# Kernel optimization log

Measured on AMD Instinct MI355X. Metric: run time of the kernel, lower is better.

## Reference

```python
import jax, jax.numpy as jnp
import numpy as np

D_EMBED = 1024
N_HEADS = 16
D_HEAD = 64
D_MLP = 4096
SEQ = 2048
BATCH = 2
ALPHA = 1.0


def setup_inputs() -> dict:
    key = jax.random.key(0)
    ks = jax.random.split(key, 7)
    s = ALPHA / np.sqrt(D_EMBED)
    return {
        "x": jax.random.normal(ks[0], (BATCH, SEQ, D_EMBED), jnp.float32),
        "W_K": s * jax.random.normal(ks[1], (N_HEADS, D_HEAD, D_EMBED), jnp.float32),
        "W_Q": s * jax.random.normal(ks[2], (N_HEADS, D_HEAD, D_EMBED), jnp.float32),
        "W_V": s * jax.random.normal(ks[3], (N_HEADS, D_HEAD, D_EMBED), jnp.float32),
        "W_O": s * jax.random.normal(ks[4], (D_EMBED, N_HEADS * D_HEAD), jnp.float32),
        "W_in": s * jax.random.normal(ks[5], (D_MLP, D_EMBED), jnp.float32),
        "b_in": jnp.zeros((D_MLP,), jnp.float32),
        "W_out": s * jax.random.normal(ks[6], (D_EMBED, D_MLP), jnp.float32),
        "b_out": jnp.zeros((D_EMBED,), jnp.float32),
    }


def reference(x, W_K, W_Q, W_V, W_O, W_in, b_in, W_out, b_out):
    b, c_len, _ = x.shape
    d_head = W_K.shape[1]
    # q/k/v: [batch, head, ctx, d_head]
    k = jnp.einsum('ahe,bce->bach', W_K, x)
    q = jnp.einsum('ahe,bce->bach', W_Q, x)
    v = jnp.einsum('ahe,bce->bach', W_V, x)
    # scores[b,a,c,C] = k_c . q_C  (faithful to original index convention)
    scores = jnp.einsum('bach,baCh->bacC', k, q)
    mask = jnp.tril(jnp.ones((c_len, c_len), dtype=x.dtype))  # [c, C]
    masked = scores * mask - 1e10 * (1.0 - mask)
    attn = jax.nn.softmax(masked / np.sqrt(d_head), axis=-1)  # softmax over C (query idx)
    # z[b,a,C,h] = sum_c v[b,a,c,h] * attn[b,a,c,C]
    z = jnp.einsum('bach,bacC->baCh', v, attn)
    z_flat = jnp.transpose(z, (0, 2, 1, 3)).reshape(b, c_len, -1)  # [b, c, a*h]
    attn_out = jnp.einsum('ef,bcf->bce', W_O, z_flat)
    x = x + attn_out
    h = jnp.einsum('me,bce->bcm', W_in, x) + b_in
    h = jax.nn.relu(h)
    mlp_out = jnp.einsum('em,bcm->bce', W_out, h) + b_out
    return x + mlp_out
```

## Files before the change

kernel.cpp:

```cpp
#include <hip/hip_runtime.h>
#include <hip/hip_bf16.h>
#include <cstdint>
#include <cstddef>

typedef __bf16 bf16;
typedef bf16 bf16x4 __attribute__((ext_vector_type(4)));
typedef bf16 bf16x8 __attribute__((ext_vector_type(8)));
typedef float floatx4 __attribute__((ext_vector_type(4)));
typedef float floatx16 __attribute__((ext_vector_type(16)));
typedef unsigned int uint;

#define MFMA16(a, b, c) __builtin_amdgcn_mfma_f32_16x16x32_bf16((a), (b), (c), 0, 0, 0)
#define MFMA32(a, b, c) __builtin_amdgcn_mfma_f32_32x32x16_bf16((a), (b), (c), 0, 0, 0)

#define K2 0.18033688011112042f

__device__ __forceinline__ void async16(const void* g, void* l) {
    __builtin_amdgcn_global_load_lds((const __attribute__((address_space(1))) void*)g,
                                     (__attribute__((address_space(3))) void*)l,
                                     16, 0, 0);
}

__device__ __forceinline__ void stage64s(const bf16* g0, int ldg, bf16* lds, int wave, int lane) {
#pragma unroll
    for (int i = 0; i < 2; ++i) {
        int r0 = wave * 16 + i * 8;
        async16(g0 + (size_t)(r0 + (lane >> 3)) * ldg + ((lane & 7) ^ (lane >> 3)) * 8,
                lds + r0 * 64);
    }
}
__device__ __forceinline__ void stage64q(const bf16* g0, int ldg, bf16* lds, int wave, int lane) {
    int r0 = wave * 8;
    async16(g0 + (size_t)(r0 + (lane >> 3)) * ldg + ((lane & 7) ^ (lane >> 3)) * 8,
            lds + r0 * 64);
}
__device__ __forceinline__ bf16x8 rd64(const bf16* t, int row, int chunk) {
    return *(const bf16x8*)&t[row * 64 + ((chunk ^ (row & 7)) * 8)];
}
__device__ __forceinline__ bf16x8 rd32(const bf16* t, int row, int quad) {
    return *(const bf16x8*)&t[row * 32 + ((quad ^ (row & 3)) * 8)];
}

__device__ __forceinline__ uint pk2(float lo, float hi) {
    union { bf16 h[2]; uint u; } c;
    c.h[0] = (bf16)lo;
    c.h[1] = (bf16)hi;
    return c.u;
}

__global__ __launch_bounds__(256) void cvt_all(const float* __restrict__ x,
                                               const float* __restrict__ WQ,
                                               const float* __restrict__ WK,
                                               const float* __restrict__ WV,
                                               const float* __restrict__ WO,
                                               const float* __restrict__ Win,
                                               const float* __restrict__ Wout,
                                               bf16* __restrict__ xb,
                                               bf16* __restrict__ wqkv,
                                               bf16* __restrict__ wo,
                                               bf16* __restrict__ win,
                                               bf16* __restrict__ wout) {
    int blk = blockIdx.x;
    const float* src;
    bf16* dst;
    int off;
    if (blk < 1024)      { src = WQ;   dst = wqkv;           off = blk; }
    else if (blk < 2048) { src = WK;   dst = wqkv + 1048576; off = blk - 1024; }
    else if (blk < 3072) { src = WV;   dst = wqkv + 2097152; off = blk - 2048; }
    else if (blk < 4096) { src = WO;   dst = wo;             off = blk - 3072; }
    else if (blk < 8192) { src = Win;  dst = win;            off = blk - 4096; }
    else if (blk < 12288){ src = Wout; dst = wout;           off = blk - 8192; }
    else                 { src = x;    dst = xb;             off = blk - 12288; }
    int i = off * 1024 + threadIdx.x * 4;
    float4 v = *(const float4*)(src + i);
    bf16x4 o = {(bf16)v.x, (bf16)v.y, (bf16)v.z, (bf16)v.w};
    *(bf16x4*)(dst + i) = o;
}

template <int EPI, int NACC>
__device__ __forceinline__ void epilogue(floatx4 (&acc)[4][NACC], int m0, int n0,
                                         int wm, int wn, int col, int quad,
                                         float* Cf, bf16* Cb, int ldc,
                                         const float* bias, const float* res) {
#pragma unroll
    for (int mi = 0; mi < 4; ++mi)
#pragma unroll
        for (int ni = 0; ni < NACC; ++ni)
#pragma unroll
            for (int r = 0; r < 4; ++r) {
                int row = m0 + wm + mi * 16 + quad * 4 + r;
                int cc = n0 + wn + ni * 16 + col;
                size_t idx = (size_t)row * ldc + cc;
                float v = acc[mi][ni][r];
                if constexpr (EPI == 0) {
                    Cb[idx] = (bf16)v;
                } else if constexpr (EPI == 1) {
                    v += res[idx];
                    Cf[idx] = v;
                    Cb[idx] = (bf16)v;
                } else if constexpr (EPI == 2) {
                    v += bias[cc];
                    v = fmaxf(v, 0.f);
                    Cb[idx] = (bf16)v;
                } else {
                    v += bias[cc] + Cf[idx];
                    Cf[idx] = v;
                }
            }
}

template <int EPI>
__global__ __launch_bounds__(256) void gemm_pipe(const bf16* __restrict__ A, int lda,
                                                 const bf16* __restrict__ B, int ldb, int K,
                                                 float* __restrict__ Cf, bf16* __restrict__ Cb,
                                                 int ldc, const float* __restrict__ bias,
                                                 const float* __restrict__ res) {
    __shared__ __align__(16) bf16 As[3][128 * 32];
    __shared__ __align__(16) bf16 Bs[3][128 * 32];
    const int tid = threadIdx.x, wave = tid >> 6, lane = tid & 63;
    const int m0 = blockIdx.y * 128, n0 = blockIdx.x * 128;
    const int wm = (wave >> 1) * 64, wn = (wave & 1) * 64;
    const int col = lane & 15, quad = lane >> 4;
    const int cs8 = ((lane & 3) ^ ((lane >> 2) & 3)) * 8;

    floatx4 acc[4][4];
#pragma unroll
    for (int mi = 0; mi < 4; ++mi)
#pragma unroll
        for (int ni = 0; ni < 4; ++ni) acc[mi][ni] = (floatx4){0.f, 0.f, 0.f, 0.f};

    auto stage = [&](int buf, int k0) {
#pragma unroll
        for (int i = 0; i < 2; ++i) {
            int r0 = wave * 32 + i * 16;
            async16(A + (size_t)(m0 + r0 + (lane >> 2)) * lda + k0 + cs8,
                    As[buf] + r0 * 32);
            async16(B + (size_t)(n0 + r0 + (lane >> 2)) * ldb + k0 + cs8,
                    Bs[buf] + r0 * 32);
        }
    };

    const int nk = K / 32;
    stage(0, 0);
    stage(1, 32);
    for (int it = 0; it < nk; ++it) {
        if (it + 1 < nk) asm volatile("s_waitcnt vmcnt(4)" ::: "memory");
        else             asm volatile("s_waitcnt vmcnt(0)" ::: "memory");
        __builtin_amdgcn_s_barrier();
        if (it + 2 < nk) stage((it + 2) % 3, (it + 2) * 32);

        const bf16* as = As[it % 3];
        const bf16* bs = Bs[it % 3];
        bf16x8 af[4], bfr[4];
#pragma unroll
        for (int mi = 0; mi < 4; ++mi) af[mi] = rd32(as, wm + mi * 16 + col, quad);
#pragma unroll
        for (int ni = 0; ni < 4; ++ni) bfr[ni] = rd32(bs, wn + ni * 16 + col, quad);
#pragma unroll
        for (int mi = 0; mi < 4; ++mi)
#pragma unroll
            for (int ni = 0; ni < 4; ++ni)
                acc[mi][ni] = MFMA16(af[mi], bfr[ni], acc[mi][ni]);
    }
    epilogue<EPI, 4>(acc, m0, n0, wm, wn, col, quad, Cf, Cb, ldc, bias, res);
}

template <int EPI>
__global__ __launch_bounds__(256) void gemm_pipe64(const bf16* __restrict__ A, int lda,
                                                   const bf16* __restrict__ B, int ldb, int K,
                                                   float* __restrict__ Cf, bf16* __restrict__ Cb,
                                                   int ldc, const float* __restrict__ bias,
                                                   const float* __restrict__ res) {
    __shared__ __align__(16) bf16 As[3][128 * 64];
    __shared__ __align__(16) bf16 Bs[3][64 * 64];
    const int tid = threadIdx.x, wave = tid >> 6, lane = tid & 63;
    const int orig = blockIdx.y * 16 + blockIdx.x;
    const int wgid = (orig & 7) * 64 + (orig >> 3);
    const int m0 = (wgid >> 4) * 128, n0 = (wgid & 15) * 64;
    const int wm = (wave >> 1) * 64, wn = (wave & 1) * 32;
    const int col = lane & 15, quad = lane >> 4;
    const int rsub = lane >> 3;
    const int csub = ((lane & 7) ^ rsub) * 8;

    floatx4 acc[4][2];
#pragma unroll
    for (int mi = 0; mi < 4; ++mi)
#pragma unroll
        for (int ni = 0; ni < 2; ++ni) acc[mi][ni] = (floatx4){0.f, 0.f, 0.f, 0.f};

    auto stage = [&](int buf, int k0) {
#pragma unroll
        for (int i = 0; i < 4; ++i) {
            int r0 = wave * 32 + i * 8;
            async16(A + (size_t)(m0 + r0 + rsub) * lda + k0 + csub, As[buf] + r0 * 64);
        }
#pragma unroll
        for (int i = 0; i < 2; ++i) {
            int r0 = wave * 16 + i * 8;
            async16(B + (size_t)(n0 + r0 + rsub) * ldb + k0 + csub, Bs[buf] + r0 * 64);
        }
    };

    const int nk = K / 64;
    stage(0, 0);
    stage(1, 64);
    for (int it = 0; it < nk; ++it) {
        if (it + 1 < nk) asm volatile("s_waitcnt vmcnt(6)" ::: "memory");
        else             asm volatile("s_waitcnt vmcnt(0)" ::: "memory");
        __builtin_amdgcn_s_barrier();
        if (it + 2 < nk) stage((it + 2) % 3, (it + 2) * 64);

        const bf16* as = As[it % 3];
        const bf16* bs = Bs[it % 3];
#pragma unroll
        for (int ks = 0; ks < 2; ++ks) {
            bf16x8 af[4], bfr[2];
#pragma unroll
            for (int mi = 0; mi < 4; ++mi) {
                int row = wm + mi * 16 + col;
                af[mi] = *(const bf16x8*)&as[row * 64 + (((ks * 4 + quad) ^ (row & 7)) * 8)];
            }
#pragma unroll
            for (int ni = 0; ni < 2; ++ni) {
                int row = wn + ni * 16 + col;
                bfr[ni] = *(const bf16x8*)&bs[row * 64 + (((ks * 4 + quad) ^ (row & 7)) * 8)];
            }
#pragma unroll
            for (int mi = 0; mi < 4; ++mi)
#pragma unroll
                for (int ni = 0; ni < 2; ++ni)
                    acc[mi][ni] = MFMA16(af[mi], bfr[ni], acc[mi][ni]);
        }
    }
    epilogue<EPI, 2>(acc, m0, n0, wm, wn, col, quad, Cf, Cb, ldc, bias, res);
}

__global__ __launch_bounds__(256) void transpose_v(const bf16* __restrict__ qkv,
                                                   const float* __restrict__ linv,
                                                   bf16* __restrict__ vt) {
    __shared__ bf16 t[64][65];
    const int bh = blockIdx.y, ct = blockIdx.x;
    const int b = bh >> 4, a = bh & 15;
    const float* lv = linv + (size_t)bh * 2048 + ct * 64;
    for (int idx = threadIdx.x; idx < 4096; idx += 256) {
        int c = idx >> 6, h = idx & 63;
        float v = (float)qkv[(size_t)(b * 2048 + ct * 64 + c) * 3072 + 2048 + a * 64 + h];
        t[h][c] = (bf16)(v * lv[c]);
    }
    __syncthreads();
    for (int idx = threadIdx.x; idx < 4096; idx += 256) {
        int h = idx >> 6, c = idx & 63;
        vt[(size_t)(bh * 64 + h) * 2048 + ct * 64 + c] = t[h][c];
    }
}

__global__ __launch_bounds__(512, 4) void attn_stats(const bf16* __restrict__ qkv,
                                                     float* __restrict__ linv) {
    __shared__ __align__(16) bf16 Kt[128 * 64];
    __shared__ __align__(16) bf16 Qt[3][64 * 64];
    __shared__ float red[4][32];
    const int xx = blockIdx.x;
    const int t = (xx & 1) ? (15 - (xx >> 1)) : (xx >> 1);
    const int bh = blockIdx.y;
    const int b = bh >> 4, a = bh & 15;
    const int tid = threadIdx.x, wave = tid >> 6, lane = tid & 63;
    const int l31 = lane & 31, lh = lane >> 5;
    const int kq = wave & 3, qh = wave >> 2;
    const bf16* base = qkv + (size_t)b * 2048 * 3072;
    const int c0 = t * 128;
    const int niter = 2 * t + 2;

    stage64s(base + (size_t)c0 * 3072 + 1024 + a * 64, 3072, Kt, wave, lane);
    stage64q(base + a * 64, 3072, Qt[0], wave, lane);
    stage64q(base + (size_t)64 * 3072 + a * 64, 3072, Qt[1], wave, lane);

    float lrun[16];
#pragma unroll
    for (int r = 0; r < 16; ++r) lrun[r] = 0.f;
    bf16x8 kf[4];

    for (int i = 0; i < niter; ++i) {
        if (i + 1 < niter) asm volatile("s_waitcnt vmcnt(1)" ::: "memory");
        else               asm volatile("s_waitcnt vmcnt(0)" ::: "memory");
        __builtin_amdgcn_s_barrier();
        if (i + 2 < niter)
            stage64q(base + (size_t)(i + 2) * 64 * 3072 + a * 64, 3072,
                     Qt[(i + 2) % 3], wave, lane);
        if (i == 0) {
#pragma unroll
            for (int s = 0; s < 4; ++s) kf[s] = rd64(Kt, 32 * kq + l31, 2 * s + lh);
        }
        const bf16* q = Qt[i % 3];
        bf16x8 qf0 = rd64(q, 32 * qh + l31, 0 + lh);
        bf16x8 qf1 = rd64(q, 32 * qh + l31, 2 + lh);
        bf16x8 qf2 = rd64(q, 32 * qh + l31, 4 + lh);
        bf16x8 qf3 = rd64(q, 32 * qh + l31, 6 + lh);
        floatx16 s0 = (floatx16)0.f, s1 = (floatx16)0.f;
        __builtin_amdgcn_s_setprio(1);
        s0 = MFMA32(kf[0], qf0, s0);
        s1 = MFMA32(kf[2], qf2, s1);
        s0 = MFMA32(kf[1], qf1, s0);
        s1 = MFMA32(kf[3], qf3, s1);
        __builtin_amdgcn_s_setprio(0);
#pragma unroll
        for (int r = 0; r < 16; ++r) {
            float e = __builtin_amdgcn_exp2f((s0[r] + s1[r]) * K2);
            if (i >= niter - 2) {
                int Crel = 64 * (i - 2 * t) + 32 * qh + l31;
                int crel = 32 * kq + (r & 3) + 8 * (r >> 2) + 4 * lh;
                if (Crel > crel) e = 0.f;
            }
            lrun[r] += e;
        }
    }
#pragma unroll
    for (int r = 0; r < 16; ++r) {
        float v = lrun[r];
        v += __shfl_xor(v, 1);
        v += __shfl_xor(v, 2);
        v += __shfl_xor(v, 4);
        v += __shfl_xor(v, 8);
        v += __shfl_xor(v, 16);
        lrun[r] = v;
    }
    if (qh == 1 && l31 == 0) {
#pragma unroll
        for (int r = 0; r < 16; ++r)
            red[kq][(r & 3) + 8 * (r >> 2) + 4 * lh] = lrun[r];
    }
    __syncthreads();
    if (qh == 0 && l31 == 0) {
#pragma unroll
        for (int r = 0; r < 16; ++r) {
            int cr = (r & 3) + 8 * (r >> 2) + 4 * lh;
            linv[(size_t)bh * 2048 + c0 + 32 * kq + cr] = 1.0f / (lrun[r] + red[kq][cr]);
        }
    }
}

__global__ __launch_bounds__(512, 4) void attn_av(const bf16* __restrict__ qkv,
                                                  const bf16* __restrict__ vt,
                                                  bf16* __restrict__ zb) {
    __shared__ __align__(16) char smem[65536];
    bf16* Qt = (bf16*)smem;
    bf16* Kt = (bf16*)(smem + 16384);
    bf16* Vt = (bf16*)(smem + 40960);
    const int xx = blockIdx.x;
    const int t = (xx & 1) ? (15 - (xx >> 1)) : (xx >> 1);
    const int bh = blockIdx.y;
    const int b = bh >> 4, a = bh & 15;
    const int tid = threadIdx.x, wave = tid >> 6, lane = tid & 63;
    const int l31 = lane & 31, lh = lane >> 5;
    const int Cq = wave & 3, cq = wave >> 2;
    const bf16* base = qkv + (size_t)b * 2048 * 3072;
    const int C0 = t * 128;
    const int niter = 32 - 2 * t;

    stage64s(base + (size_t)C0 * 3072 + a * 64, 3072, Qt, wave, lane);
    stage64q(base + (size_t)(2 * t) * 64 * 3072 + 1024 + a * 64, 3072, Kt, wave, lane);
    stage64q(vt + (size_t)bh * 64 * 2048 + 2 * t * 64, 2048, Vt, wave, lane);
    stage64q(base + (size_t)(2 * t + 1) * 64 * 3072 + 1024 + a * 64, 3072, Kt + 4096, wave, lane);
    stage64q(vt + (size_t)bh * 64 * 2048 + (2 * t + 1) * 64, 2048, Vt + 4096, wave, lane);

    floatx16 zacc[2];
    zacc[0] = (floatx16)0.f;
    zacc[1] = (floatx16)0.f;
    bf16x8 qf[4];

    for (int i = 0; i < niter; ++i) {
        const int ct = 2 * t + i;
        if (i + 1 < niter) asm volatile("s_waitcnt vmcnt(2)" ::: "memory");
        else               asm volatile("s_waitcnt vmcnt(0)" ::: "memory");
        __builtin_amdgcn_s_barrier();
        if (i + 2 < niter) {
            stage64q(base + (size_t)(ct + 2) * 64 * 3072 + 1024 + a * 64, 3072,
                     Kt + ((i + 2) % 3) * 4096, wave, lane);
            stage64q(vt + (size_t)bh * 64 * 2048 + (ct + 2) * 64, 2048,
                     Vt + ((i + 2) % 3) * 4096, wave, lane);
        }
        if (i == 0) {
#pragma unroll
            for (int s = 0; s < 4; ++s) qf[s] = rd64(Qt, 32 * Cq + l31, 2 * s + lh);
        }
        const bf16* kt = Kt + (i % 3) * 4096;
        const bf16* vts = Vt + (i % 3) * 4096;

        floatx16 s0 = (floatx16)0.f, s1 = (floatx16)0.f;
        __builtin_amdgcn_s_setprio(1);
        s0 = MFMA32(rd64(kt, 32 * cq + l31, 0 + lh), qf[0], s0);
        s1 = MFMA32(rd64(kt, 32 * cq + l31, 4 + lh), qf[2], s1);
        s0 = MFMA32(rd64(kt, 32 * cq + l31, 2 + lh), qf[1], s0);
        s1 = MFMA32(rd64(kt, 32 * cq + l31, 6 + lh), qf[3], s1);
        __builtin_amdgcn_s_setprio(0);

        float p[16];
#pragma unroll
        for (int r = 0; r < 16; ++r) {
            float e = __builtin_amdgcn_exp2f((s0[r] + s1[r]) * K2);
            if (i < 2) {
                int Crel = 32 * Cq + l31;
                int crel = 64 * i + 32 * cq + (r & 3) + 8 * (r >> 2) + 4 * lh;
                if (Crel > crel) e = 0.f;
            }
            p[r] = e;
        }

        bf16x8 pa[2];
#pragma unroll
        for (int g = 0; g < 2; ++g) {
            uint w0 = pk2(p[8 * g + 0], p[8 * g + 1]);
            uint w1 = pk2(p[8 * g + 2], p[8 * g + 3]);
            uint w2 = pk2(p[8 * g + 4], p[8 * g + 5]);
            uint w3 = pk2(p[8 * g + 6], p[8 * g + 7]);
            uint xw0 = (uint)__shfl_xor((int)w0, 32);
            uint xw1 = (uint)__shfl_xor((int)w1, 32);
            uint xw2 = (uint)__shfl_xor((int)w2, 32);
            uint xw3 = (uint)__shfl_xor((int)w3, 32);
            union { uint u[4]; bf16x8 v; } cv;
            cv.u[0] = lh ? xw2 : w0;
            cv.u[1] = lh ? xw3 : w1;
            cv.u[2] = lh ? w2 : xw0;
            cv.u[3] = lh ? w3 : xw1;
            pa[g] = cv.v;
        }

        __builtin_amdgcn_s_setprio(1);
#pragma unroll
        for (int ht = 0; ht < 2; ++ht) {
#pragma unroll
            for (int s = 0; s < 2; ++s) {
                bf16x8 vf = rd64(vts, 32 * ht + l31, 4 * cq + 2 * s + lh);
                zacc[ht] = MFMA32(pa[s], vf, zacc[ht]);
            }
        }
        __builtin_amdgcn_s_setprio(0);
    }

    __syncthreads();
    float* Zex = (float*)smem;
    if (cq == 1) {
#pragma unroll
        for (int ht = 0; ht < 2; ++ht)
#pragma unroll
            for (int q = 0; q < 4; ++q) {
                float4 t4 = {zacc[ht][4 * q + 0], zacc[ht][4 * q + 1],
                             zacc[ht][4 * q + 2], zacc[ht][4 * q + 3]};
                *(float4*)&Zex[Cq * 2048 + lane * 32 + (((ht * 4 + q) ^ (lane & 7)) * 4)] = t4;
            }
    }
    __syncthreads();
    if (cq == 0) {
#pragma unroll
        for (int ht = 0; ht < 2; ++ht)
#pragma unroll
            for (int q = 0; q < 4; ++q) {
                float4 t4 = *(const float4*)&Zex[Cq * 2048 + lane * 32 +
                                                 (((ht * 4 + q) ^ (lane & 7)) * 4)];
                zacc[ht][4 * q + 0] += t4.x;
                zacc[ht][4 * q + 1] += t4.y;
                zacc[ht][4 * q + 2] += t4.z;
                zacc[ht][4 * q + 3] += t4.w;
            }
#pragma unroll
        for (int ht = 0; ht < 2; ++ht)
#pragma unroll
            for (int r = 0; r < 16; ++r) {
                int Cg = C0 + 32 * Cq + (r & 3) + 8 * (r >> 2) + 4 * lh;
                zb[(size_t)(b * 2048 + Cg) * 1024 + a * 64 + 32 * ht + l31] =
                    (bf16)zacc[ht][r];
            }
    }
}

extern "C" void kernel_launch(void* const* d_in, const int* in_sizes, int n_in,
                              void* d_out, int out_size, void* d_ws, size_t ws_size,
                              hipStream_t stream) {
    (void)in_sizes; (void)n_in; (void)out_size; (void)ws_size;
    const float* x    = (const float*)d_in[0];
    const float* WK   = (const float*)d_in[1];
    const float* WQ   = (const float*)d_in[2];
    const float* WV   = (const float*)d_in[3];
    const float* WO   = (const float*)d_in[4];
    const float* Win  = (const float*)d_in[5];
    const float* bin  = (const float*)d_in[6];
    const float* Wout = (const float*)d_in[7];
    const float* bout = (const float*)d_in[8];
    float* out = (float*)d_out;

    char* ws = (char*)d_ws;
    bf16*  xb   = (bf16*)(ws + 0);
    bf16*  wqkv = (bf16*)(ws + 8388608);
    bf16*  wo   = (bf16*)(ws + 14680064);
    bf16*  win  = (bf16*)(ws + 16777216);
    bf16*  wout = (bf16*)(ws + 25165824);
    bf16*  qkvb = (bf16*)(ws + 33554432);
    bf16*  vtb  = (bf16*)(ws + 58720256);
    float* mst  = (float*)(ws + 67108864);
    bf16*  zbuf = (bf16*)(ws + 67633152);
    bf16*  xmid = (bf16*)(ws + 76021760);
    bf16*  hbuf = (bf16*)(ws + 84410368);

    cvt_all<<<16384, 256, 0, stream>>>(x, WQ, WK, WV, WO, Win, Wout,
                                       xb, wqkv, wo, win, wout);

    gemm_pipe<0><<<dim3(24, 32), 256, 0, stream>>>(xb, 1024, wqkv, 1024, 1024,
                                                   nullptr, qkvb, 3072, nullptr, nullptr);
    attn_stats<<<dim3(16, 32), 512, 0, stream>>>(qkvb, mst);
    transpose_v<<<dim3(32, 32), 256, 0, stream>>>(qkvb, mst, vtb);
    attn_av<<<dim3(16, 32), 512, 0, stream>>>(qkvb, vtb, zbuf);
    gemm_pipe64<1><<<dim3(16, 32), 256, 0, stream>>>(zbuf, 1024, wo, 1024, 1024,
                                                     out, xmid, 1024, nullptr, x);
    gemm_pipe<2><<<dim3(32, 32), 256, 0, stream>>>(xmid, 1024, win, 1024, 1024,
                                                   nullptr, hbuf, 4096, bin, nullptr);
    gemm_pipe64<3><<<dim3(16, 32), 256, 0, stream>>>(hbuf, 4096, wout, 4096, 4096,
                                                     out, nullptr, 1024, bout, nullptr);
}
```

Measured before the change: 380.2 us.

## Split-K the MLP down-projection GEMM with a separate reduction kernel

Replaces the final 4096-deep MLP output GEMM (128x64 tiles) with a split-K GEMM using 128x128 tiles over two K halves. Each half writes fp32 partials into workspace reused from the qkv buffer, and a small kernel sums them with the bias into the residual output. The aim is to keep enough workgroups in flight at a larger tile size for better MFMA reuse. In exchange it adds partial-buffer write/read traffic and an extra launch.

```diff
diff --git a/kernel.cpp b/kernel.cpp
--- a/kernel.cpp
+++ b/kernel.cpp
@@ -165,6 +165,89 @@
     epilogue<EPI, 4>(acc, m0, n0, wm, wn, col, quad, Cf, Cb, ldc, bias, res);
 }
 
+__global__ __launch_bounds__(256) void gemm_sk(const bf16* __restrict__ A, int lda,
+                                               const bf16* __restrict__ B, int ldb, int Kh,
+                                               float* __restrict__ P) {
+    __shared__ __align__(16) bf16 As[3][128 * 32];
+    __shared__ __align__(16) bf16 Bs[3][128 * 32];
+    const int tid = threadIdx.x, wave = tid >> 6, lane = tid & 63;
+    const int m0 = blockIdx.y * 128, n0 = blockIdx.x * 128;
+    A += (size_t)blockIdx.z * Kh;
+    B += (size_t)blockIdx.z * Kh;
+    P += (size_t)blockIdx.z * 4096 * 1024;
+    const int wm = (wave >> 1) * 64, wn = (wave & 1) * 64;
+    const int col = lane & 15, quad = lane >> 4;
+    const int cs8 = ((lane & 3) ^ ((lane >> 2) & 3)) * 8;
+
+    floatx4 acc[4][4];
+#pragma unroll
+    for (int mi = 0; mi < 4; ++mi)
+#pragma unroll
+        for (int ni = 0; ni < 4; ++ni) acc[mi][ni] = (floatx4){0.f, 0.f, 0.f, 0.f};
+
+    auto stage = [&](int buf, int k0) {
+#pragma unroll
+        for (int i = 0; i < 2; ++i) {
+            int r0 = wave * 32 + i * 16;
+            async16(A + (size_t)(m0 + r0 + (lane >> 2)) * lda + k0 + cs8,
+                    As[buf] + r0 * 32);
+            async16(B + (size_t)(n0 + r0 + (lane >> 2)) * ldb + k0 + cs8,
+                    Bs[buf] + r0 * 32);
+        }
+    };
+
+    const int nk = Kh / 32;
+    stage(0, 0);
+    stage(1, 32);
+    for (int it = 0; it < nk; ++it) {
+        if (it + 1 < nk) asm volatile("s_waitcnt vmcnt(4)" ::: "memory");
+        else             asm volatile("s_waitcnt vmcnt(0)" ::: "memory");
+        __builtin_amdgcn_s_barrier();
+        if (it + 2 < nk) stage((it + 2) % 3, (it + 2) * 32);
+
+        const bf16* as = As[it % 3];
+        const bf16* bs = Bs[it % 3];
+        bf16x8 af[4], bfr[4];
+#pragma unroll
+        for (int mi = 0; mi < 4; ++mi) af[mi] = rd32(as, wm + mi * 16 + col, quad);
+#pragma unroll
+        for (int ni = 0; ni < 4; ++ni) bfr[ni] = rd32(bs, wn + ni * 16 + col, quad);
+        __builtin_amdgcn_s_setprio(1);
+#pragma unroll
+        for (int mi = 0; mi < 4; ++mi)
+#pragma unroll
+            for (int ni = 0; ni < 4; ++ni)
+                acc[mi][ni] = MFMA16(af[mi], bfr[ni], acc[mi][ni]);
+        __builtin_amdgcn_s_setprio(0);
+    }
+#pragma unroll
+    for (int mi = 0; mi < 4; ++mi)
+#pragma unroll
+        for (int ni = 0; ni < 4; ++ni)
+#pragma unroll
+            for (int r = 0; r < 4; ++r) {
+                int row = m0 + wm + mi * 16 + quad * 4 + r;
+                int cc = n0 + wn + ni * 16 + col;
+                P[(size_t)row * 1024 + cc] = acc[mi][ni][r];
+            }
+}
+
+__global__ __launch_bounds__(256) void mlp2_reduce(const float* __restrict__ p0,
+                                                   const float* __restrict__ p1,
+                                                   const float* __restrict__ bout,
+                                                   float* __restrict__ out) {
+    int i = (blockIdx.x * 256 + threadIdx.x) * 4;
+    float4 a = *(const float4*)(p0 + i);
+    float4 b = *(const float4*)(p1 + i);
+    float4 o = *(const float4*)(out + i);
+    float4 bb = *(const float4*)(bout + (i & 1023));
+    o.x += a.x + b.x + bb.x;
+    o.y += a.y + b.y + bb.y;
+    o.z += a.z + b.z + bb.z;
+    o.w += a.w + b.w + bb.w;
+    *(float4*)(out + i) = o;
+}
+
 template <int EPI>
 __global__ __launch_bounds__(256) void gemm_pipe64(const bf16* __restrict__ A, int lda,
                                                    const bf16* __restrict__ B, int ldb, int K,
@@ -499,6 +582,7 @@
     bf16*  zbuf = (bf16*)(ws + 67633152);
     bf16*  xmid = (bf16*)(ws + 76021760);
     bf16*  hbuf = (bf16*)(ws + 84410368);
+    float* part = (float*)(ws + 33554432);
 
     cvt_all<<<16384, 256, 0, stream>>>(x, WQ, WK, WV, WO, Win, Wout,
                                        xb, wqkv, wo, win, wout);
@@ -512,6 +596,6 @@
                                                      out, xmid, 1024, nullptr, x);
     gemm_pipe<2><<<dim3(32, 32), 256, 0, stream>>>(xmid, 1024, win, 1024, 1024,
                                                    nullptr, hbuf, 4096, bin, nullptr);
-    gemm_pipe64<3><<<dim3(16, 32), 256, 0, stream>>>(hbuf, 4096, wout, 4096, 4096,
-                                                     out, nullptr, 1024, bout, nullptr);
-}
+    gemm_sk<<<dim3(8, 32, 2), 256, 0, stream>>>(hbuf, 4096, wout, 4096, 2048, part);
+    mlp2_reduce<<<4096, 256, 0, stream>>>(part, part + 4194304, bout, out);
+}
```

Result: no change. 380.4 us (+0.1%).
